# Kernel optimization log

Measured on AMD Instinct MI355X. Metric: run time of the kernel, lower is better.

The kernel has to match this reference:

```python
import jax, jax.numpy as jnp
import numpy as np

B, N, IN_DIM, OUT_DIM = 8, 2048, 128, 64
TEMPERATURE = 1.0
NEG_SLOPE = 0.2


def setup_inputs() -> dict:
    key = jax.random.key(0)
    k1, k2, k3, k4, k5 = jax.random.split(key, 5)
    s_fc = 1.0 / np.sqrt(IN_DIM)
    s_at = 1.0 / np.sqrt(2 * OUT_DIM)
    return {
        "h": jax.random.normal(k1, (B, N, IN_DIM), dtype=jnp.float32),
        "W_fc": jax.random.normal(k2, (IN_DIM, OUT_DIM), dtype=jnp.float32) * s_fc,
        "b_fc": jax.random.normal(k3, (OUT_DIM,), dtype=jnp.float32) * s_fc,
        "a_src": jax.random.normal(k4, (OUT_DIM,), dtype=jnp.float32) * s_at,
        "a_dst": jax.random.normal(k5, (OUT_DIM,), dtype=jnp.float32) * s_at,
        "b_attn": jnp.zeros((), dtype=jnp.float32),
    }


def reference(h, W_fc, b_fc, a_src, a_dst, b_attn):
    # hp: (B, N, OUT_DIM) -- projected node features
    hp = h @ W_fc + b_fc
    # attn_fc(concat(h_i, h_j)) == h_i@a_src + h_j@a_dst + b (exact decomposition)
    s = hp @ a_src  # (B, N) source contribution
    d = hp @ a_dst  # (B, N) dest contribution
    scores = s[:, :, None] + d[:, None, :] + b_attn  # (B, N, N)
    scores = jnp.where(scores >= 0, scores, NEG_SLOPE * scores)  # leaky_relu
    scores = scores / TEMPERATURE
    attn = jax.nn.softmax(scores, axis=-1)
    out = jnp.einsum("bij,bjd->bid", attn, hp)
    return jax.nn.elu(out)
```

## Files before the change

kernel.cpp:

```cpp
#include <hip/hip_runtime.h>
#include <math.h>

#define BB 8
#define NN 2048
#define IND 128
#define OUTD 64
#define NEG 0.2f

typedef __attribute__((ext_vector_type(4))) float f32x4;
typedef __attribute__((ext_vector_type(2))) _Float16 h2;
typedef __attribute__((ext_vector_type(8))) _Float16 half8;

__device__ __forceinline__ unsigned short f2h(float f) {
    union { _Float16 h; unsigned short u; } c;
    c.h = (_Float16)f;
    return c.u;
}

__global__ __launch_bounds__(512) void gat_proj_kernel(
    const float* __restrict__ h, const float* __restrict__ W,
    const float* __restrict__ bfc, const float* __restrict__ asrc,
    const float* __restrict__ adst,
    unsigned short* __restrict__ hpT2, float* __restrict__ s,
    _Float16* __restrict__ F, _Float16* __restrict__ H)
{
    __shared__ float Wl[IND * OUTD];
    __shared__ float hl[64 * 132];

    const int t  = threadIdx.x;
    const int R0 = blockIdx.x * 64;

    const float4* W4 = (const float4*)W;
    float4*       Wl4 = (float4*)Wl;
    #pragma unroll
    for (int k2 = 0; k2 < 4; ++k2) Wl4[t + k2 * 512] = W4[t + k2 * 512];

    const float4* h4 = (const float4*)(h + (size_t)R0 * IND);
    #pragma unroll
    for (int k2 = 0; k2 < 4; ++k2) {
        const int idx = t + k2 * 512;
        const int row = idx >> 5, c4 = idx & 31;
        *(float4*)&hl[row * 132 + c4 * 4] = h4[idx];
    }
    __syncthreads();

    const int r0 = (t >> 4) * 2;
    const int o0 = (t & 15) * 4;
    const float4 bias = *(const float4*)(bfc + o0);
    float4 a0 = bias, a1 = bias;

    #pragma unroll 2
    for (int kc = 0; kc < IND; kc += 4) {
        const float4 w0 = *(const float4*)&Wl[(kc + 0) * OUTD + o0];
        const float4 w1 = *(const float4*)&Wl[(kc + 1) * OUTD + o0];
        const float4 w2 = *(const float4*)&Wl[(kc + 2) * OUTD + o0];
        const float4 w3 = *(const float4*)&Wl[(kc + 3) * OUTD + o0];
        const float4 h0 = *(const float4*)&hl[(r0 + 0) * 132 + kc];
        const float4 h1 = *(const float4*)&hl[(r0 + 1) * 132 + kc];

        a0.x = fmaf(h0.x, w0.x, a0.x); a0.y = fmaf(h0.x, w0.y, a0.y);
        a0.z = fmaf(h0.x, w0.z, a0.z); a0.w = fmaf(h0.x, w0.w, a0.w);
        a0.x = fmaf(h0.y, w1.x, a0.x); a0.y = fmaf(h0.y, w1.y, a0.y);
        a0.z = fmaf(h0.y, w1.z, a0.z); a0.w = fmaf(h0.y, w1.w, a0.w);
        a0.x = fmaf(h0.z, w2.x, a0.x); a0.y = fmaf(h0.z, w2.y, a0.y);
        a0.z = fmaf(h0.z, w2.z, a0.z); a0.w = fmaf(h0.z, w2.w, a0.w);
        a0.x = fmaf(h0.w, w3.x, a0.x); a0.y = fmaf(h0.w, w3.y, a0.y);
        a0.z = fmaf(h0.w, w3.z, a0.z); a0.w = fmaf(h0.w, w3.w, a0.w);

        a1.x = fmaf(h1.x, w0.x, a1.x); a1.y = fmaf(h1.x, w0.y, a1.y);
        a1.z = fmaf(h1.x, w0.z, a1.z); a1.w = fmaf(h1.x, w0.w, a1.w);
        a1.x = fmaf(h1.y, w1.x, a1.x); a1.y = fmaf(h1.y, w1.y, a1.y);
        a1.z = fmaf(h1.y, w1.z, a1.z); a1.w = fmaf(h1.y, w1.w, a1.w);
        a1.x = fmaf(h1.z, w2.x, a1.x); a1.y = fmaf(h1.z, w2.y, a1.y);
        a1.z = fmaf(h1.z, w2.z, a1.z); a1.w = fmaf(h1.z, w2.w, a1.w);
        a1.x = fmaf(h1.w, w3.x, a1.x); a1.y = fmaf(h1.w, w3.y, a1.y);
        a1.z = fmaf(h1.w, w3.z, a1.z); a1.w = fmaf(h1.w, w3.w, a1.w);
    }

    const int b   = R0 >> 11;
    const int jb0 = (R0 & 2047) + r0;
    const int cj  = jb0 >> 3;
    const int sub = jb0 & 7;
    unsigned short* cbase = hpT2 + (((size_t)(b * 256 + cj)) * OUTD) * 8;
    {
        ushort2 v;
        v.x = f2h(a0.x); v.y = f2h(a1.x);
        *(ushort2*)(cbase + (o0 + 0) * 8 + sub) = v;
        v.x = f2h(a0.y); v.y = f2h(a1.y);
        *(ushort2*)(cbase + (o0 + 1) * 8 + sub) = v;
        v.x = f2h(a0.z); v.y = f2h(a1.z);
        *(ushort2*)(cbase + (o0 + 2) * 8 + sub) = v;
        v.x = f2h(a0.w); v.y = f2h(a1.w);
        *(ushort2*)(cbase + (o0 + 3) * 8 + sub) = v;
    }

    const float4 as4 = *(const float4*)(asrc + o0);
    const float4 ad4 = *(const float4*)(adst + o0);
    float vs[2], vd[2];
    vs[0] = a0.x*as4.x + a0.y*as4.y + a0.z*as4.z + a0.w*as4.w;
    vs[1] = a1.x*as4.x + a1.y*as4.y + a1.z*as4.z + a1.w*as4.w;
    vd[0] = a0.x*ad4.x + a0.y*ad4.y + a0.z*ad4.z + a0.w*ad4.w;
    vd[1] = a1.x*ad4.x + a1.y*ad4.y + a1.z*ad4.z + a1.w*ad4.w;
    #pragma unroll
    for (int msk = 1; msk <= 8; msk <<= 1) {
        vs[0] += __shfl_xor(vs[0], msk);
        vs[1] += __shfl_xor(vs[1], msk);
        vd[0] += __shfl_xor(vd[0], msk);
        vd[1] += __shfl_xor(vd[1], msk);
    }
    if ((t & 15) == 0) {
        #pragma unroll
        for (int r = 0; r < 2; ++r) {
            s[R0 + r0 + r] = vs[r];
            F[R0 + r0 + r] = (_Float16)__expf(vd[r]);
            H[R0 + r0 + r] = (_Float16)__expf(NEG * vd[r]);
        }
    }
}

__global__ __launch_bounds__(512) void gat_attn_kernel(
    const unsigned short* __restrict__ hpT2, const float* __restrict__ s,
    const _Float16* __restrict__ F, const _Float16* __restrict__ H,
    const float* __restrict__ battn_p, float* __restrict__ out)
{
    __shared__ float accl[4][64 * 66];
    __shared__ float ll[8][64];

    const int t    = threadIdx.x;
    const int lane = t & 63;
    const int wv   = t >> 6;
    const int blk  = blockIdx.x;
    const int b    = blk >> 5;
    const int i0   = (blk & 31) * 64;
    const int m    = lane & 15;
    const int kc   = lane >> 4;

    const float battn = battn_p[0];
    h2 E2[4], G2[4];
    #pragma unroll
    for (int T = 0; T < 4; ++T) {
        const float smv = s[b * NN + i0 + T * 16 + m] + battn;
        const float Ef = __expf(smv);
        const float Gf = __expf(NEG * smv);
        E2[T] = (h2){(_Float16)Ef, (_Float16)Ef};
        G2[T] = (h2){(_Float16)Gf, (_Float16)Gf};
    }
    const _Float16* Fb = F + b * NN;
    const _Float16* Hb = H + b * NN;
    const _Float16* hb = (const _Float16*)hpT2 + (size_t)b * 256 * OUTD * 8;

    half8 ones;
    #pragma unroll
    for (int q = 0; q < 8; ++q) ones[q] = (_Float16)1.0f;

    f32x4 acc[4][4];
    f32x4 dacc[4];
    #pragma unroll
    for (int T = 0; T < 4; ++T) {
        dacc[T] = (f32x4){0.f, 0.f, 0.f, 0.f};
        #pragma unroll
        for (int ot = 0; ot < 4; ++ot) acc[T][ot] = (f32x4){0.f, 0.f, 0.f, 0.f};
    }

    const int jbase = wv * (NN / 8);

    #pragma unroll 2
    for (int it = 0; it < NN / 8 / 32; ++it) {
        const int j0 = jbase + it * 32;
        const size_t cb = ((size_t)((j0 >> 3) + kc)) * OUTD * 8;
        const half8 bf0 = *(const half8*)(hb + cb + (0 * 16 + m) * 8);
        const half8 bf1 = *(const half8*)(hb + cb + (1 * 16 + m) * 8);
        const half8 bf2 = *(const half8*)(hb + cb + (2 * 16 + m) * 8);
        const half8 bf3 = *(const half8*)(hb + cb + (3 * 16 + m) * 8);

        union { float4 q; h2 p[4]; } Ff, Hf;
        Ff.q = *(const float4*)(Fb + j0 + kc * 8);
        Hf.q = *(const float4*)(Hb + j0 + kc * 8);

        #pragma unroll
        for (int T = 0; T < 4; ++T) {
            union { half8 v; h2 p[4]; } af;
            af.p[0] = __builtin_elementwise_max(E2[T] * Ff.p[0], G2[T] * Hf.p[0]);
            af.p[1] = __builtin_elementwise_max(E2[T] * Ff.p[1], G2[T] * Hf.p[1]);
            af.p[2] = __builtin_elementwise_max(E2[T] * Ff.p[2], G2[T] * Hf.p[2]);
            af.p[3] = __builtin_elementwise_max(E2[T] * Ff.p[3], G2[T] * Hf.p[3]);

            acc[T][0] = __builtin_amdgcn_mfma_f32_16x16x32_f16(af.v, bf0, acc[T][0], 0, 0, 0);
            acc[T][1] = __builtin_amdgcn_mfma_f32_16x16x32_f16(af.v, bf1, acc[T][1], 0, 0, 0);
            acc[T][2] = __builtin_amdgcn_mfma_f32_16x16x32_f16(af.v, bf2, acc[T][2], 0, 0, 0);
            acc[T][3] = __builtin_amdgcn_mfma_f32_16x16x32_f16(af.v, bf3, acc[T][3], 0, 0, 0);
            dacc[T]   = __builtin_amdgcn_mfma_f32_16x16x32_f16(af.v, ones, dacc[T], 0, 0, 0);
        }
    }

    if (m == 0) {
        #pragma unroll
        for (int T = 0; T < 4; ++T)
            #pragma unroll
            for (int r = 0; r < 4; ++r) ll[wv][T * 16 + kc * 4 + r] = dacc[T][r];
    }

    if (wv >= 4) {
        #pragma unroll
        for (int T = 0; T < 4; ++T) {
            #pragma unroll
            for (int r = 0; r < 4; ++r) {
                const int row = T * 16 + kc * 4 + r;
                accl[wv - 4][row * 66 + 0 * 16 + m] = acc[T][0][r];
                accl[wv - 4][row * 66 + 1 * 16 + m] = acc[T][1][r];
                accl[wv - 4][row * 66 + 2 * 16 + m] = acc[T][2][r];
                accl[wv - 4][row * 66 + 3 * 16 + m] = acc[T][3][r];
            }
        }
    }
    __syncthreads();
    if (wv < 4) {
        #pragma unroll
        for (int T = 0; T < 4; ++T) {
            #pragma unroll
            for (int r = 0; r < 4; ++r) {
                const int row = T * 16 + kc * 4 + r;
                accl[wv][row * 66 + 0 * 16 + m] += acc[T][0][r];
                accl[wv][row * 66 + 1 * 16 + m] += acc[T][1][r];
                accl[wv][row * 66 + 2 * 16 + m] += acc[T][2][r];
                accl[wv][row * 66 + 3 * 16 + m] += acc[T][3][r];
            }
        }
    }
    __syncthreads();

    const int col = t & 63;
    const int r0e = (t >> 6) * 8;
    float* ob = out + (((size_t)b * NN + i0) * OUTD);
    #pragma unroll 4
    for (int r = 0; r < 8; ++r) {
        const int row = r0e + r;
        const float lsum = ((ll[0][row] + ll[1][row]) + (ll[2][row] + ll[3][row])) +
                           ((ll[4][row] + ll[5][row]) + (ll[6][row] + ll[7][row]));
        float v = (accl[0][row * 66 + col] + accl[1][row * 66 + col]) +
                  (accl[2][row * 66 + col] + accl[3][row * 66 + col]);
        v /= lsum;
        v = (v > 0.f) ? v : expm1f(v);
        ob[(size_t)row * OUTD + col] = v;
    }
}

extern "C" void kernel_launch(void* const* d_in, const int* in_sizes, int n_in,
                              void* d_out, int out_size, void* d_ws, size_t ws_size,
                              hipStream_t stream)
{
    const float* h     = (const float*)d_in[0];
    const float* W     = (const float*)d_in[1];
    const float* bfc   = (const float*)d_in[2];
    const float* asrc  = (const float*)d_in[3];
    const float* adst  = (const float*)d_in[4];
    const float* battn = (const float*)d_in[5];
    float* out = (float*)d_out;

    unsigned short* hpT2 = (unsigned short*)d_ws;
    float*     s = (float*)((char*)d_ws + (size_t)BB * NN * OUTD * 2);
    _Float16*  F = (_Float16*)(s + (size_t)BB * NN);
    _Float16*  H = F + (size_t)BB * NN;

    gat_proj_kernel<<<(BB * NN) / 64, 512, 0, stream>>>(h, W, bfc, asrc, adst,
                                                        hpT2, s, F, H);
    gat_attn_kernel<<<BB * (NN / 64), 512, 0, stream>>>(hpT2, s, F, H, battn, out);
}
```

Baseline: 83.98 us.

## Compute projection GEMM with split-fp16 MFMA instead of scalar FMAs

Rewrites the projection kernel to use 16x16x32 f16 MFMA instructions. Each fp32 operand is split into hi and lo fp16 parts and three MFMAs are issued per step to keep near-fp32 accuracy. W is transposed into LDS as fp16 hi/lo, h is loaded straight into registers, and the s/d reductions now combine across two waves through LDS with an extra barrier. This replaces the scalar FMA loop on the projection stage, which is small next to the attention kernel.

```diff
diff --git a/kernel.cpp b/kernel.cpp
--- a/kernel.cpp
+++ b/kernel.cpp
@@ -24,97 +24,132 @@
     unsigned short* __restrict__ hpT2, float* __restrict__ s,
     _Float16* __restrict__ F, _Float16* __restrict__ H)
 {
-    __shared__ float Wl[IND * OUTD];
-    __shared__ float hl[64 * 132];
-
-    const int t  = threadIdx.x;
-    const int R0 = blockIdx.x * 64;
+    __shared__ _Float16 WtH[64 * 136];
+    __shared__ _Float16 WtL[64 * 136];
+    __shared__ float sps[64][2];
+    __shared__ float spd[64][2];
+
+    const int t    = threadIdx.x;
+    const int lane = t & 63;
+    const int wv   = t >> 6;
+    const int R0   = blockIdx.x * 64;
 
     const float4* W4 = (const float4*)W;
-    float4*       Wl4 = (float4*)Wl;
-    #pragma unroll
-    for (int k2 = 0; k2 < 4; ++k2) Wl4[t + k2 * 512] = W4[t + k2 * 512];
-
-    const float4* h4 = (const float4*)(h + (size_t)R0 * IND);
-    #pragma unroll
-    for (int k2 = 0; k2 < 4; ++k2) {
-        const int idx = t + k2 * 512;
-        const int row = idx >> 5, c4 = idx & 31;
-        *(float4*)&hl[row * 132 + c4 * 4] = h4[idx];
-    }
+    #pragma unroll
+    for (int i = 0; i < 4; ++i) {
+        const int idx = t + i * 512;
+        union { float4 q; float f[4]; } w;
+        w.q = W4[idx];
+        const int k  = idx >> 4;
+        const int o0 = (idx & 15) * 4;
+        #pragma unroll
+        for (int c = 0; c < 4; ++c) {
+            const float v = w.f[c];
+            const _Float16 hi = (_Float16)v;
+            const _Float16 lo = (_Float16)(v - (float)hi);
+            WtH[(o0 + c) * 136 + k] = hi;
+            WtL[(o0 + c) * 136 + k] = lo;
+        }
+    }
+
+    const int rt = wv >> 1;
+    const int nh = wv & 1;
+    const int m  = lane & 15;
+    const int g  = lane >> 4;
+
+    const int o_0 = nh * 32 + m;
+    const int o_1 = nh * 32 + 16 + m;
+
+    const float* hrow = h + (size_t)(R0 + rt * 16 + m) * IND + g * 8;
+    half8 ahi[4], alo[4];
+    #pragma unroll
+    for (int ks = 0; ks < 4; ++ks) {
+        union { float4 q; float f[4]; } p0, p1;
+        p0.q = *(const float4*)(hrow + ks * 32);
+        p1.q = *(const float4*)(hrow + ks * 32 + 4);
+        #pragma unroll
+        for (int e = 0; e < 4; ++e) {
+            const _Float16 hi0 = (_Float16)p0.f[e];
+            ahi[ks][e] = hi0;
+            alo[ks][e] = (_Float16)(p0.f[e] - (float)hi0);
+            const _Float16 hi1 = (_Float16)p1.f[e];
+            ahi[ks][4 + e] = hi1;
+            alo[ks][4 + e] = (_Float16)(p1.f[e] - (float)hi1);
+        }
+    }
+
+    f32x4 acc0, acc1;
+    {
+        const float b0 = bfc[o_0], b1 = bfc[o_1];
+        acc0 = (f32x4){b0, b0, b0, b0};
+        acc1 = (f32x4){b1, b1, b1, b1};
+    }
+
     __syncthreads();
 
-    const int r0 = (t >> 4) * 2;
-    const int o0 = (t & 15) * 4;
-    const float4 bias = *(const float4*)(bfc + o0);
-    float4 a0 = bias, a1 = bias;
-
-    #pragma unroll 2
-    for (int kc = 0; kc < IND; kc += 4) {
-        const float4 w0 = *(const float4*)&Wl[(kc + 0) * OUTD + o0];
-        const float4 w1 = *(const float4*)&Wl[(kc + 1) * OUTD + o0];
-        const float4 w2 = *(const float4*)&Wl[(kc + 2) * OUTD + o0];
-        const float4 w3 = *(const float4*)&Wl[(kc + 3) * OUTD + o0];
-        const float4 h0 = *(const float4*)&hl[(r0 + 0) * 132 + kc];
-        const float4 h1 = *(const float4*)&hl[(r0 + 1) * 132 + kc];
-
-        a0.x = fmaf(h0.x, w0.x, a0.x); a0.y = fmaf(h0.x, w0.y, a0.y);
-        a0.z = fmaf(h0.x, w0.z, a0.z); a0.w = fmaf(h0.x, w0.w, a0.w);
-        a0.x = fmaf(h0.y, w1.x, a0.x); a0.y = fmaf(h0.y, w1.y, a0.y);
-        a0.z = fmaf(h0.y, w1.z, a0.z); a0.w = fmaf(h0.y, w1.w, a0.w);
-        a0.x = fmaf(h0.z, w2.x, a0.x); a0.y = fmaf(h0.z, w2.y, a0.y);
-        a0.z = fmaf(h0.z, w2.z, a0.z); a0.w = fmaf(h0.z, w2.w, a0.w);
-        a0.x = fmaf(h0.w, w3.x, a0.x); a0.y = fmaf(h0.w, w3.y, a0.y);
-        a0.z = fmaf(h0.w, w3.z, a0.z); a0.w = fmaf(h0.w, w3.w, a0.w);
-
-        a1.x = fmaf(h1.x, w0.x, a1.x); a1.y = fmaf(h1.x, w0.y, a1.y);
-        a1.z = fmaf(h1.x, w0.z, a1.z); a1.w = fmaf(h1.x, w0.w, a1.w);
-        a1.x = fmaf(h1.y, w1.x, a1.x); a1.y = fmaf(h1.y, w1.y, a1.y);
-        a1.z = fmaf(h1.y, w1.z, a1.z); a1.w = fmaf(h1.y, w1.w, a1.w);
-        a1.x = fmaf(h1.z, w2.x, a1.x); a1.y = fmaf(h1.z, w2.y, a1.y);
-        a1.z = fmaf(h1.z, w2.z, a1.z); a1.w = fmaf(h1.z, w2.w, a1.w);
-        a1.x = fmaf(h1.w, w3.x, a1.x); a1.y = fmaf(h1.w, w3.y, a1.y);
-        a1.z = fmaf(h1.w, w3.z, a1.z); a1.w = fmaf(h1.w, w3.w, a1.w);
+    #pragma unroll
+    for (int ks = 0; ks < 4; ++ks) {
+        const int kb = ks * 32 + g * 8;
+        const half8 bh0 = *(const half8*)&WtH[o_0 * 136 + kb];
+        const half8 bl0 = *(const half8*)&WtL[o_0 * 136 + kb];
+        const half8 bh1 = *(const half8*)&WtH[o_1 * 136 + kb];
+        const half8 bl1 = *(const half8*)&WtL[o_1 * 136 + kb];
+
+        acc0 = __builtin_amdgcn_mfma_f32_16x16x32_f16(ahi[ks], bh0, acc0, 0, 0, 0);
+        acc0 = __builtin_amdgcn_mfma_f32_16x16x32_f16(ahi[ks], bl0, acc0, 0, 0, 0);
+        acc0 = __builtin_amdgcn_mfma_f32_16x16x32_f16(alo[ks], bh0, acc0, 0, 0, 0);
+
+        acc1 = __builtin_amdgcn_mfma_f32_16x16x32_f16(ahi[ks], bh1, acc1, 0, 0, 0);
+        acc1 = __builtin_amdgcn_mfma_f32_16x16x32_f16(ahi[ks], bl1, acc1, 0, 0, 0);
+        acc1 = __builtin_amdgcn_mfma_f32_16x16x32_f16(alo[ks], bh1, acc1, 0, 0, 0);
     }
 
     const int b   = R0 >> 11;
-    const int jb0 = (R0 & 2047) + r0;
+    const int jb0 = (R0 & 2047) + rt * 16 + g * 4;
     const int cj  = jb0 >> 3;
     const int sub = jb0 & 7;
     unsigned short* cbase = hpT2 + (((size_t)(b * 256 + cj)) * OUTD) * 8;
     {
-        ushort2 v;
-        v.x = f2h(a0.x); v.y = f2h(a1.x);
-        *(ushort2*)(cbase + (o0 + 0) * 8 + sub) = v;
-        v.x = f2h(a0.y); v.y = f2h(a1.y);
-        *(ushort2*)(cbase + (o0 + 1) * 8 + sub) = v;
-        v.x = f2h(a0.z); v.y = f2h(a1.z);
-        *(ushort2*)(cbase + (o0 + 2) * 8 + sub) = v;
-        v.x = f2h(a0.w); v.y = f2h(a1.w);
-        *(ushort2*)(cbase + (o0 + 3) * 8 + sub) = v;
-    }
-
-    const float4 as4 = *(const float4*)(asrc + o0);
-    const float4 ad4 = *(const float4*)(adst + o0);
-    float vs[2], vd[2];
-    vs[0] = a0.x*as4.x + a0.y*as4.y + a0.z*as4.z + a0.w*as4.w;
-    vs[1] = a1.x*as4.x + a1.y*as4.y + a1.z*as4.z + a1.w*as4.w;
-    vd[0] = a0.x*ad4.x + a0.y*ad4.y + a0.z*ad4.z + a0.w*ad4.w;
-    vd[1] = a1.x*ad4.x + a1.y*ad4.y + a1.z*ad4.z + a1.w*ad4.w;
+        ushort4 u;
+        u.x = f2h(acc0[0]); u.y = f2h(acc0[1]);
+        u.z = f2h(acc0[2]); u.w = f2h(acc0[3]);
+        *(ushort4*)(cbase + o_0 * 8 + sub) = u;
+        u.x = f2h(acc1[0]); u.y = f2h(acc1[1]);
+        u.z = f2h(acc1[2]); u.w = f2h(acc1[3]);
+        *(ushort4*)(cbase + o_1 * 8 + sub) = u;
+    }
+
+    const float a_s0 = asrc[o_0], a_s1 = asrc[o_1];
+    const float a_d0 = adst[o_0], a_d1 = adst[o_1];
+    float ps[4], pd[4];
+    #pragma unroll
+    for (int r = 0; r < 4; ++r) {
+        ps[r] = acc0[r] * a_s0 + acc1[r] * a_s1;
+        pd[r] = acc0[r] * a_d0 + acc1[r] * a_d1;
+    }
     #pragma unroll
     for (int msk = 1; msk <= 8; msk <<= 1) {
-        vs[0] += __shfl_xor(vs[0], msk);
-        vs[1] += __shfl_xor(vs[1], msk);
-        vd[0] += __shfl_xor(vd[0], msk);
-        vd[1] += __shfl_xor(vd[1], msk);
-    }
-    if ((t & 15) == 0) {
-        #pragma unroll
-        for (int r = 0; r < 2; ++r) {
-            s[R0 + r0 + r] = vs[r];
-            F[R0 + r0 + r] = (_Float16)__expf(vd[r]);
-            H[R0 + r0 + r] = (_Float16)__expf(NEG * vd[r]);
-        }
+        #pragma unroll
+        for (int r = 0; r < 4; ++r) {
+            ps[r] += __shfl_xor(ps[r], msk);
+            pd[r] += __shfl_xor(pd[r], msk);
+        }
+    }
+    if (m == 0) {
+        #pragma unroll
+        for (int r = 0; r < 4; ++r) {
+            const int row = rt * 16 + g * 4 + r;
+            sps[row][nh] = ps[r];
+            spd[row][nh] = pd[r];
+        }
+    }
+    __syncthreads();
+    if (t < 64) {
+        const float sv = sps[t][0] + sps[t][1];
+        const float dv = spd[t][0] + spd[t][1];
+        s[R0 + t] = sv;
+        F[R0 + t] = (_Float16)__expf(dv);
+        H[R0 + t] = (_Float16)__expf(NEG * dv);
     }
 }
 
```

Measured after the change: 81.40 us. -3.1%, faster.
